# Kernel tuning notes

Hardware: AMD Instinct MI355X
Metric: run time of the kernel (lower is better)

The kernel has to match this reference:

```python
import jax, jax.numpy as jnp
import numpy as np

N_FFT = 512
N_STAGES = 4
BASE = N_FFT >> N_STAGES          # base DFT size = 32
SPLIT0 = N_FFT // 2 + 1           # rfft bins = 257
BATCH = 32768


def _mod_seq(order):
    # bit-reversed offset sequence used by get_partial_bit_reversal_matrix
    mset = [0]
    for o in range(order):
        step = 2 ** o
        mset = [v for x in mset for v in (x, x + step)]
    return mset


def _perm_indices():
    # gather indices equivalent to the partial bit-reversal permutation matmul
    base = 2 ** N_STAGES
    n_per = N_FFT // base
    idx = []
    for p in _mod_seq(N_STAGES):
        idx.extend(j * base + p for j in range(n_per))
    return np.asarray(idx, dtype=np.int32)

_PERM_IDX = _perm_indices()
_DFT = np.fft.fft(np.eye(BASE))   # symmetric DFT matrix, M[j,k]=exp(-2pi i jk/BASE)


def setup_inputs() -> dict:
    key = jax.random.key(0)
    x = jax.random.normal(key, (BATCH, N_FFT), dtype=jnp.float32)
    return {"x": x}


def reference(x):
    dt = x.dtype
    dft_r = jnp.asarray(_DFT.real, dtype=dt)
    dft_i = jnp.asarray(_DFT.imag, dtype=dt)

    B = x.shape[0]
    # partial bit-reversal permutation (FFTPermuter) as a gather
    y = x[..., _PERM_IDX].reshape(B, 2 ** N_STAGES, BASE)
    ev = y[:, ::2]   # even-decimated sub-sequences (B, 2^(s-1), BASE)
    od = y[:, 1::2]  # odd-decimated  sub-sequences

    # base-case DFT (DFT module): x @ M with symmetric M
    ev_r = jnp.einsum('bml,lk->bmk', ev, dft_r)
    ev_i = jnp.einsum('bml,lk->bmk', ev, dft_i)
    od_r = jnp.einsum('bml,lk->bmk', od, dft_r)
    od_i = jnp.einsum('bml,lk->bmk', od, dft_i)

    # radix-2 butterfly combine stages (FFTwiddle with SIMPLE ops)
    L = BASE
    for _ in range(N_STAGES):
        w = np.exp(-2j * np.pi * np.arange(L) / (2 * L))
        tw_r = jnp.asarray(w.real, dtype=dt)
        tw_i = jnp.asarray(w.imag, dtype=dt)
        todd_r = tw_r * od_r - tw_i * od_i
        todd_i = tw_r * od_i + tw_i * od_r
        real = jnp.concatenate([ev_r + todd_r, ev_r - todd_r], axis=-1)
        imag = jnp.concatenate([ev_i + todd_i, ev_i - todd_i], axis=-1)
        ev_r, od_r = real[:, ::2], real[:, 1::2]
        ev_i, od_i = imag[:, ::2], imag[:, 1::2]
        L *= 2

    # rfft truncation (torch.split in _RFFTDecompWithGMAC)
    yre = ev_r[:, 0, :SPLIT0]
    yim = ev_i[:, 0, :SPLIT0]
    return (yre, yim)
```

## Files before the change

### kernel.cpp

```cpp
#include <hip/hip_runtime.h>


#define NFFT 512
#define MC   256
#define WPB  4
#define PAD(i) ((i) + ((i) >> 5))

__device__ __forceinline__ void r4stage(
    const float* __restrict__ sr, const float* __restrict__ si,
    float* __restrict__ dr, float* __restrict__ di,
    int t, int p, int wbase, int ws, float invn)
{
    float ar = sr[PAD(t)],       ai = si[PAD(t)];
    float br = sr[PAD(t + 64)],  bi = si[PAD(t + 64)];
    float cr = sr[PAD(t + 128)], ci = si[PAD(t + 128)];
    float er = sr[PAD(t + 192)], ei = si[PAD(t + 192)];

    float apcr = ar + cr, apci = ai + ci;
    float amcr = ar - cr, amci = ai - ci;
    float bpdr = br + er, bpdi = bi + ei;
    float bmdr = br - er, bmdi = bi - ei;

    float y0r = apcr + bpdr, y0i = apci + bpdi;
    float u1r = amcr + bmdi, u1i = amci - bmdr;
    float u2r = apcr - bpdr, u2i = apci - bpdi;
    float u3r = amcr - bmdi, u3i = amci + bmdr;

    float ang = -6.28318530717958647692f * (float)p * invn;
    float sn, cs;
    __sincosf(ang, &sn, &cs);
    float w1r = cs, w1i = sn;
    float w2r = cs * cs - sn * sn, w2i = 2.0f * cs * sn;
    float w3r = w1r * w2r - w1i * w2i, w3i = w1r * w2i + w1i * w2r;

    dr[PAD(wbase)]          = y0r;
    di[PAD(wbase)]          = y0i;
    dr[PAD(wbase + ws)]     = w1r * u1r - w1i * u1i;
    di[PAD(wbase + ws)]     = w1r * u1i + w1i * u1r;
    dr[PAD(wbase + 2 * ws)] = w2r * u2r - w2i * u2i;
    di[PAD(wbase + 2 * ws)] = w2r * u2i + w2i * u2r;
    dr[PAD(wbase + 3 * ws)] = w3r * u3r - w3i * u3i;
    di[PAD(wbase + 3 * ws)] = w3r * u3i + w3i * u3r;
}

__global__ __launch_bounds__(256) void rfft512_kernel(
    const float* __restrict__ x, float* __restrict__ out, int batch)
{
    __shared__ float lds[WPB][4][264];
    const int t = threadIdx.x & 63;
    const int w = threadIdx.x >> 6;
    long long b = (long long)blockIdx.x * WPB + w;
    if (b >= batch) b = batch - 1;

    float* re0 = lds[w][0];
    float* im0 = lds[w][1];
    float* re1 = lds[w][2];
    float* im1 = lds[w][3];

    const float4* xf4 = (const float4*)(x + b * NFFT);
    float4 v0 = xf4[t];
    float4 v1 = xf4[t + 64];
    re0[PAD(2 * t)]       = v0.x;  im0[PAD(2 * t)]       = v0.y;
    re0[PAD(2 * t + 1)]   = v0.z;  im0[PAD(2 * t + 1)]   = v0.w;
    re0[PAD(2 * t + 128)] = v1.x;  im0[PAD(2 * t + 128)] = v1.y;
    re0[PAD(2 * t + 129)] = v1.z;  im0[PAD(2 * t + 129)] = v1.w;
    __syncthreads();

    r4stage(re0, im0, re1, im1, t, t, 4 * t, 1, 1.0f / 256.0f);
    __syncthreads();
    r4stage(re1, im1, re0, im0, t, t >> 2, (t & 3) + 16 * (t >> 2), 4, 1.0f / 64.0f);
    __syncthreads();
    r4stage(re0, im0, re1, im1, t, t >> 4, (t & 15) + 64 * (t >> 4), 16, 1.0f / 16.0f);
    __syncthreads();
    r4stage(re1, im1, re0, im0, t, 0, t, 64, 1.0f / 4.0f);
    __syncthreads();

    float* outRe = out + b * 257;
    float* outIm = out + (long long)batch * 257 + b * 257;
#pragma unroll
    for (int j = 0; j < 4; ++j) {
        int k = t + 64 * j;
        int km = (MC - k) & (MC - 1);
        float zr = re0[PAD(k)],  zi = im0[PAD(k)];
        float pr = re0[PAD(km)], pi = im0[PAD(km)];
        float Ar = 0.5f * (zr + pr);
        float Ai = 0.5f * (zi - pi);
        float Br = 0.5f * (zi + pi);
        float Bi = -0.5f * (zr - pr);
        float ang = -6.28318530717958647692f * (float)k * (1.0f / 512.0f);
        float sn, cs;
        __sincosf(ang, &sn, &cs);
        outRe[k] = Ar + cs * Br - sn * Bi;
        outIm[k] = Ai + cs * Bi + sn * Br;
    }
    if (t == 0) {
        float zr = re0[PAD(0)], zi = im0[PAD(0)];
        outRe[256] = zr - zi;
        outIm[256] = 0.0f;
    }
}

extern "C" void kernel_launch(void* const* d_in, const int* in_sizes, int n_in,
                              void* d_out, int out_size, void* d_ws, size_t ws_size,
                              hipStream_t stream)
{
    const float* x = (const float*)d_in[0];
    float* out = (float*)d_out;
    const int batch = in_sizes[0] / NFFT;
    const int grid = (batch + WPB - 1) / WPB;
    rfft512_kernel<<<grid, 256, 0, stream>>>(x, out, batch);
}
```

Baseline: 110.5 us.

## Use interleaved float2 LDS with XOR swizzle and wave-level sync in rfft512

Replaces the separate padded real and imaginary LDS arrays with interleaved float2 buffers indexed through an XOR swizzle, so loads and stores become vectorised float2/float4 accesses. Each wavefront owns its own FFT, so the block-wide __syncthreads barriers are replaced by an lgkmcnt wait. The final stage keeps its outputs in registers and only writes them back for the mirrored-index reads. This cuts LDS instruction count and barrier stalls. The risk is that relying on the LDS wait alone as intra-wave ordering is fragile if the compiler reorders accesses.

New measurement: 109.1 us. About the same (-1.3%).

```diff
diff --git a/kernel.cpp b/kernel.cpp
--- a/kernel.cpp
+++ b/kernel.cpp
@@ -2,100 +2,149 @@
 
 
 #define NFFT 512
-#define MC   256
 #define WPB  4
-#define PAD(i) ((i) + ((i) >> 5))
 
-__device__ __forceinline__ void r4stage(
-    const float* __restrict__ sr, const float* __restrict__ si,
-    float* __restrict__ dr, float* __restrict__ di,
-    int t, int p, int wbase, int ws, float invn)
-{
-    float ar = sr[PAD(t)],       ai = si[PAD(t)];
-    float br = sr[PAD(t + 64)],  bi = si[PAD(t + 64)];
-    float cr = sr[PAD(t + 128)], ci = si[PAD(t + 128)];
-    float er = sr[PAD(t + 192)], ei = si[PAD(t + 192)];
+__device__ __forceinline__ int SW(int i) { return i ^ ((i >> 2) & 12); }
 
-    float apcr = ar + cr, apci = ai + ci;
-    float amcr = ar - cr, amci = ai - ci;
-    float bpdr = br + er, bpdi = bi + ei;
-    float bmdr = br - er, bmdi = bi - ei;
-
-    float y0r = apcr + bpdr, y0i = apci + bpdi;
-    float u1r = amcr + bmdi, u1i = amci - bmdr;
-    float u2r = apcr - bpdr, u2i = apci - bpdi;
-    float u3r = amcr - bmdi, u3i = amci + bmdr;
-
-    float ang = -6.28318530717958647692f * (float)p * invn;
-    float sn, cs;
-    __sincosf(ang, &sn, &cs);
-    float w1r = cs, w1i = sn;
-    float w2r = cs * cs - sn * sn, w2i = 2.0f * cs * sn;
-    float w3r = w1r * w2r - w1i * w2i, w3i = w1r * w2i + w1i * w2r;
-
-    dr[PAD(wbase)]          = y0r;
-    di[PAD(wbase)]          = y0i;
-    dr[PAD(wbase + ws)]     = w1r * u1r - w1i * u1i;
-    di[PAD(wbase + ws)]     = w1r * u1i + w1i * u1r;
-    dr[PAD(wbase + 2 * ws)] = w2r * u2r - w2i * u2i;
-    di[PAD(wbase + 2 * ws)] = w2r * u2i + w2i * u2r;
-    dr[PAD(wbase + 3 * ws)] = w3r * u3r - w3i * u3i;
-    di[PAD(wbase + 3 * ws)] = w3r * u3i + w3i * u3r;
+__device__ __forceinline__ void waveSyncLds() {
+    asm volatile("s_waitcnt lgkmcnt(0)" ::: "memory");
 }
 
 __global__ __launch_bounds__(256) void rfft512_kernel(
     const float* __restrict__ x, float* __restrict__ out, int batch)
 {
-    __shared__ float lds[WPB][4][264];
+    __shared__ __align__(16) float2 lds[WPB][2][256];
     const int t = threadIdx.x & 63;
     const int w = threadIdx.x >> 6;
     long long b = (long long)blockIdx.x * WPB + w;
     if (b >= batch) b = batch - 1;
 
-    float* re0 = lds[w][0];
-    float* im0 = lds[w][1];
-    float* re1 = lds[w][2];
-    float* im1 = lds[w][3];
+    float2* buf0 = lds[w][0];
+    float2* buf1 = lds[w][1];
 
     const float4* xf4 = (const float4*)(x + b * NFFT);
     float4 v0 = xf4[t];
     float4 v1 = xf4[t + 64];
-    re0[PAD(2 * t)]       = v0.x;  im0[PAD(2 * t)]       = v0.y;
-    re0[PAD(2 * t + 1)]   = v0.z;  im0[PAD(2 * t + 1)]   = v0.w;
-    re0[PAD(2 * t + 128)] = v1.x;  im0[PAD(2 * t + 128)] = v1.y;
-    re0[PAD(2 * t + 129)] = v1.z;  im0[PAD(2 * t + 129)] = v1.w;
-    __syncthreads();
+    {
+        int p0 = SW(2 * t);
+        float4* b4 = (float4*)buf0;
+        b4[p0 >> 1]        = v0;
+        b4[(p0 >> 1) + 64] = v1;
+    }
+    waveSyncLds();
 
-    r4stage(re0, im0, re1, im1, t, t, 4 * t, 1, 1.0f / 256.0f);
-    __syncthreads();
-    r4stage(re1, im1, re0, im0, t, t >> 2, (t & 3) + 16 * (t >> 2), 4, 1.0f / 64.0f);
-    __syncthreads();
-    r4stage(re0, im0, re1, im1, t, t >> 4, (t & 15) + 64 * (t >> 4), 16, 1.0f / 16.0f);
-    __syncthreads();
-    r4stage(re1, im1, re0, im0, t, 0, t, 64, 1.0f / 4.0f);
-    __syncthreads();
+    const float NEG2PI = -6.28318530717958647692f;
+
+    {
+        int rb = SW(t);
+        float2 a = buf0[rb], bb = buf0[rb + 64], c = buf0[rb + 128], d = buf0[rb + 192];
+        float apcr = a.x + c.x, apci = a.y + c.y;
+        float amcr = a.x - c.x, amci = a.y - c.y;
+        float bpdr = bb.x + d.x, bpdi = bb.y + d.y;
+        float bmdr = bb.x - d.x, bmdi = bb.y - d.y;
+        float y0r = apcr + bpdr, y0i = apci + bpdi;
+        float u1r = amcr + bmdi, u1i = amci - bmdr;
+        float u2r = apcr - bpdr, u2i = apci - bpdi;
+        float u3r = amcr - bmdi, u3i = amci + bmdr;
+        float sn, cs;
+        __sincosf(NEG2PI * (float)t * (1.0f / 256.0f), &sn, &cs);
+        float w1r = cs, w1i = sn;
+        float w2r = cs * cs - sn * sn, w2i = 2.0f * cs * sn;
+        float w3r = w1r * w2r - w1i * w2i, w3i = w1r * w2i + w1i * w2r;
+        int wb = (4 * t) ^ (t & 12);
+        float4* d4 = (float4*)buf1;
+        d4[wb >> 1]       = make_float4(y0r, y0i,
+                                        w1r * u1r - w1i * u1i, w1r * u1i + w1i * u1r);
+        d4[(wb >> 1) + 1] = make_float4(w2r * u2r - w2i * u2i, w2r * u2i + w2i * u2r,
+                                        w3r * u3r - w3i * u3i, w3r * u3i + w3i * u3r);
+    }
+    waveSyncLds();
+
+    {
+        int rb = SW(t);
+        float2 a = buf1[rb], bb = buf1[rb + 64], c = buf1[rb + 128], d = buf1[rb + 192];
+        float apcr = a.x + c.x, apci = a.y + c.y;
+        float amcr = a.x - c.x, amci = a.y - c.y;
+        float bpdr = bb.x + d.x, bpdi = bb.y + d.y;
+        float bmdr = bb.x - d.x, bmdi = bb.y - d.y;
+        float y0r = apcr + bpdr, y0i = apci + bpdi;
+        float u1r = amcr + bmdi, u1i = amci - bmdr;
+        float u2r = apcr - bpdr, u2i = apci - bpdi;
+        float u3r = amcr - bmdi, u3i = amci + bmdr;
+        float sn, cs;
+        __sincosf(NEG2PI * (float)(t >> 2) * (1.0f / 64.0f), &sn, &cs);
+        float w1r = cs, w1i = sn;
+        float w2r = cs * cs - sn * sn, w2i = 2.0f * cs * sn;
+        float w3r = w1r * w2r - w1i * w2i, w3i = w1r * w2i + w1i * w2r;
+        int wbase = (t & 3) + 16 * (t >> 2);
+        buf0[SW(wbase)]      = make_float2(y0r, y0i);
+        buf0[SW(wbase + 4)]  = make_float2(w1r * u1r - w1i * u1i, w1r * u1i + w1i * u1r);
+        buf0[SW(wbase + 8)]  = make_float2(w2r * u2r - w2i * u2i, w2r * u2i + w2i * u2r);
+        buf0[SW(wbase + 12)] = make_float2(w3r * u3r - w3i * u3i, w3r * u3i + w3i * u3r);
+    }
+    waveSyncLds();
+
+    {
+        int rb = SW(t);
+        float2 a = buf0[rb], bb = buf0[rb + 64], c = buf0[rb + 128], d = buf0[rb + 192];
+        float apcr = a.x + c.x, apci = a.y + c.y;
+        float amcr = a.x - c.x, amci = a.y - c.y;
+        float bpdr = bb.x + d.x, bpdi = bb.y + d.y;
+        float bmdr = bb.x - d.x, bmdi = bb.y - d.y;
+        float y0r = apcr + bpdr, y0i = apci + bpdi;
+        float u1r = amcr + bmdi, u1i = amci - bmdr;
+        float u2r = apcr - bpdr, u2i = apci - bpdi;
+        float u3r = amcr - bmdi, u3i = amci + bmdr;
+        float sn, cs;
+        __sincosf(NEG2PI * (float)(t >> 4) * (1.0f / 16.0f), &sn, &cs);
+        float w1r = cs, w1i = sn;
+        float w2r = cs * cs - sn * sn, w2i = 2.0f * cs * sn;
+        float w3r = w1r * w2r - w1i * w2i, w3i = w1r * w2i + w1i * w2r;
+        int wbase = (t & 15) + 64 * (t >> 4);
+        buf1[SW(wbase)]      = make_float2(y0r, y0i);
+        buf1[SW(wbase + 16)] = make_float2(w1r * u1r - w1i * u1i, w1r * u1i + w1i * u1r);
+        buf1[SW(wbase + 32)] = make_float2(w2r * u2r - w2i * u2i, w2r * u2i + w2i * u2r);
+        buf1[SW(wbase + 48)] = make_float2(w3r * u3r - w3i * u3i, w3r * u3i + w3i * u3r);
+    }
+    waveSyncLds();
+
+    float zr[4], zi[4];
+    {
+        int rb = SW(t);
+        float2 a = buf1[rb], bb = buf1[rb + 64], c = buf1[rb + 128], d = buf1[rb + 192];
+        float apcr = a.x + c.x, apci = a.y + c.y;
+        float amcr = a.x - c.x, amci = a.y - c.y;
+        float bpdr = bb.x + d.x, bpdi = bb.y + d.y;
+        float bmdr = bb.x - d.x, bmdi = bb.y - d.y;
+        zr[0] = apcr + bpdr; zi[0] = apci + bpdi;
+        zr[1] = amcr + bmdi; zi[1] = amci - bmdr;
+        zr[2] = apcr - bpdr; zi[2] = apci - bpdi;
+        zr[3] = amcr - bmdi; zi[3] = amci + bmdr;
+        buf0[rb]       = make_float2(zr[0], zi[0]);
+        buf0[rb + 64]  = make_float2(zr[1], zi[1]);
+        buf0[rb + 128] = make_float2(zr[2], zi[2]);
+        buf0[rb + 192] = make_float2(zr[3], zi[3]);
+    }
+    waveSyncLds();
 
     float* outRe = out + b * 257;
     float* outIm = out + (long long)batch * 257 + b * 257;
 #pragma unroll
     for (int j = 0; j < 4; ++j) {
         int k = t + 64 * j;
-        int km = (MC - k) & (MC - 1);
-        float zr = re0[PAD(k)],  zi = im0[PAD(k)];
-        float pr = re0[PAD(km)], pi = im0[PAD(km)];
-        float Ar = 0.5f * (zr + pr);
-        float Ai = 0.5f * (zi - pi);
-        float Br = 0.5f * (zi + pi);
-        float Bi = -0.5f * (zr - pr);
-        float ang = -6.28318530717958647692f * (float)k * (1.0f / 512.0f);
+        int km = (256 - k) & 255;
+        float2 pm = buf0[SW(km)];
+        float Ar = 0.5f * (zr[j] + pm.x);
+        float Ai = 0.5f * (zi[j] - pm.y);
+        float Br = 0.5f * (zi[j] + pm.y);
+        float Bi = -0.5f * (zr[j] - pm.x);
         float sn, cs;
-        __sincosf(ang, &sn, &cs);
+        __sincosf(NEG2PI * (float)k * (1.0f / 512.0f), &sn, &cs);
         outRe[k] = Ar + cs * Br - sn * Bi;
         outIm[k] = Ai + cs * Bi + sn * Br;
     }
     if (t == 0) {
-        float zr = re0[PAD(0)], zi = im0[PAD(0)];
-        outRe[256] = zr - zi;
+        outRe[256] = zr[0] - zi[0];
         outIm[256] = 0.0f;
     }
 }
```
